# Kernel tuning notes

Hardware: AMD Instinct MI355X
Metric: run time of the kernel (lower is better)

## Reference

```python
import jax, jax.numpy as jnp
import numpy as np

LEAK = 0.9
BASE_THRESH = 1.0
BN_EPS = 1e-5

@jax.custom_vjp
def spike_fn(x):
    return (x >= 0).astype(x.dtype)

def _spike_fwd(x):
    return (x >= 0).astype(x.dtype), x

def _spike_bwd(x, g):
    return (g / (1.0 + 5.0 * jnp.abs(x)) ** 2,)

spike_fn.defvjp(_spike_fwd, _spike_bwd)


def setup_inputs() -> dict:
    key = jax.random.key(0)
    ks = jax.random.split(key, 8)
    B, T, C, H, NC, DT = 256, 2048, 64, 64, 4, 50
    kin_spikes_seq = jax.random.normal(ks[0], (B, T, C), dtype=jnp.float32)
    tda_features = jax.random.normal(ks[1], (B, DT), dtype=jnp.float32)
    # spatial_conv1x1: Linear(64 -> 64, bias=False); weight [out, in]
    W_spatial = jax.random.normal(ks[2], (H, C), dtype=jnp.float32) / np.sqrt(C)
    bn_gamma = jnp.ones((H,), dtype=jnp.float32)
    bn_beta = jnp.zeros((H,), dtype=jnp.float32)
    # class_conv1x1: Linear(64 -> 4, bias=False)
    W_class = jax.random.normal(ks[3], (NC, H), dtype=jnp.float32) / np.sqrt(H)
    lateral = jnp.eye(NC, dtype=jnp.float32) * 0.8 - 0.1
    # tda_to_thresh: Linear(50 -> 4)
    W_tda = jax.random.normal(ks[4], (NC, DT), dtype=jnp.float32) / np.sqrt(DT)
    b_tda = jnp.zeros((NC,), dtype=jnp.float32)
    return {
        "kin_spikes_seq": kin_spikes_seq,
        "tda_features": tda_features,
        "W_spatial": W_spatial,
        "bn_gamma": bn_gamma,
        "bn_beta": bn_beta,
        "W_class": W_class,
        "lateral": lateral,
        "W_tda": W_tda,
        "b_tda": b_tda,
    }


def reference(kin_spikes_seq, tda_features, W_spatial, bn_gamma, bn_beta,
              W_class, lateral, W_tda, b_tda):
    # [B, T, C] @ [C, H] -> [B, T, H]
    x_proj = jnp.einsum("btc,hc->bth", kin_spikes_seq, W_spatial)
    # BatchNorm1d in training mode: per-channel stats over (B, T)
    mean = jnp.mean(x_proj, axis=(0, 1))
    var = jnp.var(x_proj, axis=(0, 1))
    x_proj = (x_proj - mean) * jax.lax.rsqrt(var + BN_EPS) * bn_gamma + bn_beta

    tda_mod = jax.nn.sigmoid(tda_features @ W_tda.T + b_tda) * 0.5  # [B, 4]
    dynamic_thresh = BASE_THRESH + tda_mod

    B = kin_spikes_seq.shape[0]
    H, NC = W_class.shape[1], W_class.shape[0]
    mem1 = jnp.zeros((B, H), dtype=x_proj.dtype)
    mem2 = jnp.zeros((B, NC), dtype=x_proj.dtype)
    spike_sum = jnp.zeros((B, NC), dtype=x_proj.dtype)

    def step(carry, xt):
        mem1, mem2, ssum = carry
        mem1 = LEAK * mem1 + xt
        spk1 = spike_fn(mem1 - BASE_THRESH)
        mem1 = mem1 * (1.0 - spk1)
        cur2 = (spk1 @ W_class.T) @ lateral  # [B, 4]
        mem2 = LEAK * mem2 + cur2
        spk2 = spike_fn(mem2 - dynamic_thresh)
        mem2 = mem2 * (1.0 - spk2)
        return (mem1, mem2, ssum + spk2), None

    xs = jnp.swapaxes(x_proj, 0, 1)  # [T, B, H]
    (mem1, mem2, spike_sum), _ = jax.lax.scan(step, (mem1, mem2, spike_sum), xs)
    return spike_sum
```

## Files before the change

### kernel.cpp

```cpp
#include <hip/hip_runtime.h>
#include <cstdint>
#include <cstddef>
#include <cmath>

#define BB 256
#define TB 2048
#define NROWS (BB*TB)
#define R1 256
#define NBLK_K1 (NROWS/R1)
#define NBLK1 4096

typedef float f32x4 __attribute__((ext_vector_type(4)));
typedef float f32x2 __attribute__((ext_vector_type(2)));

#define OFF_X      0ull
#define SZ_X       ((size_t)NROWS*64*4)
#define OFF_PART   (OFF_X + SZ_X)
#define SZ_PART    ((size_t)128*NBLK1*4)
#define OFF_STAT   (OFF_PART + SZ_PART)
#define SZ_STAT    (128*8)

__global__ __launch_bounds__(256, 2) void k1_gemm(const float* __restrict__ kin,
                                                  const float* __restrict__ Wsp,
                                                  float* __restrict__ xproj,
                                                  float* __restrict__ partials) {
  __shared__ float4 As[R1 * 16];
  __shared__ f32x4 Wp[32 * 32];
  const int tid = threadIdx.x;
  const int ty = tid >> 3;
  const int tx = tid & 7;
  const size_t r0 = (size_t)blockIdx.x * R1;

  const f32x4* kin4 = (const f32x4*)(kin + r0 * 64);
  #pragma unroll
  for (int k = 0; k < 16; ++k) {
    int idx = k * 256 + tid;
    int r = idx >> 4, cc = idx & 15;
    f32x4 v = __builtin_nontemporal_load(&kin4[idx]);
    As[r * 16 + (cc ^ ((r >> 3) & 7))] = make_float4(v.x, v.y, v.z, v.w);
  }
  #pragma unroll
  for (int k = 0; k < 4; ++k) {
    int idx = k * 256 + tid;
    int p = idx >> 5, q = idx & 31;
    float2 w0 = *(const float2*)(Wsp + (2 * p) * 64 + 2 * q);
    float2 w1 = *(const float2*)(Wsp + (2 * p + 1) * 64 + 2 * q);
    Wp[p * 32 + (q ^ ((p >> 2) & 7))] = (f32x4){w0.x, w1.x, w0.y, w1.y};
  }
  __syncthreads();

  f32x2 acc2[8][4];
  #pragma unroll
  for (int i = 0; i < 8; ++i)
    #pragma unroll
    for (int jp = 0; jp < 4; ++jp) acc2[i][jp] = (f32x2){0.f, 0.f};

  #pragma unroll 1
  for (int cc = 0; cc < 16; ++cc) {
    float4 av[8];
    f32x4 q0[4], q1[4];
    #pragma unroll
    for (int i = 0; i < 8; ++i)
      av[i] = As[(8 * ty + i) * 16 + (cc ^ (ty & 7))];
    #pragma unroll
    for (int jp = 0; jp < 4; ++jp) {
      const int p = 4 * tx + jp;
      q0[jp] = Wp[p * 32 + ((2 * cc)     ^ tx)];
      q1[jp] = Wp[p * 32 + ((2 * cc + 1) ^ tx)];
    }
    #pragma unroll
    for (int i = 0; i < 8; ++i) {
      #pragma unroll
      for (int jp = 0; jp < 4; ++jp) {
        acc2[i][jp] = __builtin_elementwise_fma((f32x2){av[i].x, av[i].x}, q0[jp].xy, acc2[i][jp]);
        acc2[i][jp] = __builtin_elementwise_fma((f32x2){av[i].y, av[i].y}, q0[jp].zw, acc2[i][jp]);
        acc2[i][jp] = __builtin_elementwise_fma((f32x2){av[i].z, av[i].z}, q1[jp].xy, acc2[i][jp]);
        acc2[i][jp] = __builtin_elementwise_fma((f32x2){av[i].w, av[i].w}, q1[jp].zw, acc2[i][jp]);
      }
    }
  }

  #pragma unroll
  for (int i = 0; i < 8; ++i) {
    const size_t row = r0 + 8 * ty + i;
    f32x4 lo = {acc2[i][0].x, acc2[i][0].y, acc2[i][1].x, acc2[i][1].y};
    f32x4 hi = {acc2[i][2].x, acc2[i][2].y, acc2[i][3].x, acc2[i][3].y};
    *(f32x4*)(xproj + row * 64 + 8 * tx)     = lo;
    *(f32x4*)(xproj + row * 64 + 8 * tx + 4) = hi;
  }

  __syncthreads();
  float* Sm = (float*)As;
  float* Sq = Sm + 64 * 33;
  #pragma unroll
  for (int j = 0; j < 8; ++j) {
    const int col = 8 * tx + j;
    float s = 0.f, q = 0.f;
    #pragma unroll
    for (int i = 0; i < 8; ++i) {
      float v = (j & 1) ? acc2[i][j >> 1].y : acc2[i][j >> 1].x;
      s += v;
      q += v * v;
    }
    Sm[col * 33 + ty] = s;
    Sq[col * 33 + ty] = q;
  }
  __syncthreads();
  if (tid < 64) {
    float s0 = 0.f, q0 = 0.f, s1 = 0.f, q1 = 0.f;
    #pragma unroll
    for (int g = 0; g < 16; ++g)  { s0 += Sm[tid * 33 + g]; q0 += Sq[tid * 33 + g]; }
    #pragma unroll
    for (int g = 16; g < 32; ++g) { s1 += Sm[tid * 33 + g]; q1 += Sq[tid * 33 + g]; }
    const size_t p0 = 2 * (size_t)blockIdx.x;
    partials[(size_t)tid * NBLK1 + p0]            = s0;
    partials[(size_t)tid * NBLK1 + p0 + 1]        = s1;
    partials[(size_t)(64 + tid) * NBLK1 + p0]     = q0;
    partials[(size_t)(64 + tid) * NBLK1 + p0 + 1] = q1;
  }
}

__global__ __launch_bounds__(256) void k2a_reduce(const float* __restrict__ partials,
                                                  double* __restrict__ statd) {
  __shared__ double sd[256];
  const int idx = blockIdx.x;
  double acc = 0.0;
  for (int k = threadIdx.x; k < NBLK1; k += 256)
    acc += (double)partials[(size_t)idx * NBLK1 + k];
  sd[threadIdx.x] = acc;
  __syncthreads();
  for (int s = 128; s > 0; s >>= 1) {
    if (threadIdx.x < s) sd[threadIdx.x] += sd[threadIdx.x + s];
    __syncthreads();
  }
  if (threadIdx.x == 0) statd[idx] = sd[0];
}

#define K3_LOAD(BUF, TBASE)                         \
  { _Pragma("unroll") for (int i_ = 0; i_ < 64; ++i_) \
      BUF[i_] = xr[(size_t)((TBASE) + i_) * 64]; }

#define K3_CHUNK(CUR, NXT0, TBASE)                                   \
  { unsigned long long keep = 0;                                     \
    _Pragma("unroll") for (int i_ = 0; i_ < 64; ++i_) {              \
      bool sp = (mem >= 1.0f);                                       \
      unsigned long long mb = __ballot(sp);                          \
      if (h == i_) keep = mb;                                        \
      float xrn = (i_ < 63) ? CUR[(i_ + 1) & 63] : (NXT0);           \
      float xn = fmaf(xrn, sc, sh);                                  \
      mem = sp ? xn : fmaf(mem, 0.9f, xn);                           \
    }                                                                \
    masksL[(TBASE) + h] = keep; }

#define K45_LOAD(BUF, TBASE)                                             \
  { _Pragma("unroll") for (int k_ = 0; k_ < 16; ++k_) {                  \
      f32x4 v = *(const f32x4*)(cr + (TBASE) + 4 * k_);                  \
      BUF[4 * k_] = v.x; BUF[4 * k_ + 1] = v.y;                          \
      BUF[4 * k_ + 2] = v.z; BUF[4 * k_ + 3] = v.w; } }

#define K45_CHUNK(CUR, NXT0)                                  \
  { _Pragma("unroll") for (int i_ = 0; i_ < 64; ++i_) {       \
      bool sp = (mem2 >= th);                                 \
      cnt += sp ? 1u : 0u;                                    \
      float xn = (i_ < 63) ? CUR[(i_ + 1) & 63] : (NXT0);     \
      mem2 = sp ? xn : fmaf(mem2, 0.9f, xn);                  \
    } }

__global__ __launch_bounds__(256) void k345_scan(const float* __restrict__ xproj,
                                                 const double* __restrict__ statd,
                                                 const float* __restrict__ gamma,
                                                 const float* __restrict__ beta,
                                                 const float* __restrict__ Wc,
                                                 const float* __restrict__ lat,
                                                 const float* __restrict__ tda,
                                                 const float* __restrict__ Wtda,
                                                 const float* __restrict__ btda,
                                                 float* __restrict__ out) {
  __shared__ unsigned long long masksL[TB];
  __shared__ float WcL[256];
  __shared__ float latL[16];
  __shared__ float thL[4];
  __shared__ float lbuf[4][TB + 4];
  const int tid = threadIdx.x, b = blockIdx.x;

  WcL[tid] = Wc[tid];
  if (tid < 16) latL[tid] = lat[tid];

  if (tid < 64) {
    const int h = tid;
    const double mean = statd[h] / (double)NROWS;
    const double ex2  = statd[64 + h] / (double)NROWS;
    const double var  = ex2 - mean * mean;
    const double scd  = (double)gamma[h] / sqrt(var + 1e-5);
    const float sc = (float)scd;
    const float sh = (float)((double)beta[h] - mean * scd);

    const float* xr = xproj + (size_t)b * TB * 64 + h;
    float xa[64], xb[64];

    K3_LOAD(xa, 0)
    float mem = fmaf(xa[0], sc, sh);

    #pragma unroll 1
    for (int t0 = 0; t0 < TB; t0 += 128) {
      K3_LOAD(xb, t0 + 64)
      K3_CHUNK(xa, xb[0], t0)
      if (t0 + 128 < TB) { K3_LOAD(xa, t0 + 128) }
      K3_CHUNK(xb, xa[0], t0 + 64)
    }
  } else if (tid < 68) {
    const int j = tid - 64;
    double acc = (double)btda[j];
    for (int k = 0; k < 50; ++k)
      acc += (double)tda[b * 50 + k] * (double)Wtda[j * 50 + k];
    double sig = 1.0 / (1.0 + exp(-acc));
    thL[j] = (float)(1.0 + 0.5 * sig);
  }
  __syncthreads();

  #pragma unroll 1
  for (int c = 0; c < 8; ++c) {
    const int t = c * 256 + tid;
    const unsigned long long m = masksL[t];
    const unsigned lo = (unsigned)m, hi = (unsigned)(m >> 32);
    float v0 = 0.f, v1 = 0.f, v2 = 0.f, v3 = 0.f;
    #pragma unroll
    for (int hh = 0; hh < 32; ++hh) {
      const float bit = (float)((lo >> hh) & 1u);
      v0 = fmaf(bit, WcL[hh],       v0);
      v1 = fmaf(bit, WcL[64 + hh],  v1);
      v2 = fmaf(bit, WcL[128 + hh], v2);
      v3 = fmaf(bit, WcL[192 + hh], v3);
    }
    #pragma unroll
    for (int hh = 32; hh < 64; ++hh) {
      const float bit = (float)((hi >> (hh - 32)) & 1u);
      v0 = fmaf(bit, WcL[hh],       v0);
      v1 = fmaf(bit, WcL[64 + hh],  v1);
      v2 = fmaf(bit, WcL[128 + hh], v2);
      v3 = fmaf(bit, WcL[192 + hh], v3);
    }
    { float cx = v0 * latL[0];  cx = fmaf(v1, latL[4],  cx); cx = fmaf(v2, latL[8],  cx); cx = fmaf(v3, latL[12], cx); lbuf[0][t] = cx; }
    { float cx = v0 * latL[1];  cx = fmaf(v1, latL[5],  cx); cx = fmaf(v2, latL[9],  cx); cx = fmaf(v3, latL[13], cx); lbuf[1][t] = cx; }
    { float cx = v0 * latL[2];  cx = fmaf(v1, latL[6],  cx); cx = fmaf(v2, latL[10], cx); cx = fmaf(v3, latL[14], cx); lbuf[2][t] = cx; }
    { float cx = v0 * latL[3];  cx = fmaf(v1, latL[7],  cx); cx = fmaf(v2, latL[11], cx); cx = fmaf(v3, latL[15], cx); lbuf[3][t] = cx; }
  }
  __syncthreads();
  if (tid >= 64) return;

  const int j4 = tid & 3;
  const float th = thL[j4];
  const float* cr = lbuf[j4];
  float ca[64], cb[64];

  K45_LOAD(ca, 0)
  float mem2 = ca[0];
  unsigned cnt = 0;

  #pragma unroll 1
  for (int t0 = 0; t0 < TB; t0 += 128) {
    K45_LOAD(cb, t0 + 64)
    K45_CHUNK(ca, cb[0])
    if (t0 + 128 < TB) { K45_LOAD(ca, t0 + 128) }
    K45_CHUNK(cb, ca[0])
  }
  if (tid < 4) out[b * 4 + j4] = (float)cnt;
}

extern "C" void kernel_launch(void* const* d_in, const int* in_sizes, int n_in,
                              void* d_out, int out_size, void* d_ws, size_t ws_size,
                              hipStream_t stream) {
  const float* kin   = (const float*)d_in[0];
  const float* tda   = (const float*)d_in[1];
  const float* Wsp   = (const float*)d_in[2];
  const float* gamma = (const float*)d_in[3];
  const float* beta  = (const float*)d_in[4];
  const float* Wc    = (const float*)d_in[5];
  const float* lat   = (const float*)d_in[6];
  const float* Wtda  = (const float*)d_in[7];
  const float* btda  = (const float*)d_in[8];

  char* ws = (char*)d_ws;
  float*  xproj    = (float*)(ws + OFF_X);
  float*  partials = (float*)(ws + OFF_PART);
  double* statd    = (double*)(ws + OFF_STAT);
  float*  out      = (float*)d_out;

  k1_gemm  <<<dim3(NBLK_K1), dim3(256), 0, stream>>>(kin, Wsp, xproj, partials);
  k2a_reduce<<<dim3(128),  dim3(256), 0, stream>>>(partials, statd);
  k345_scan<<<dim3(BB),    dim3(256), 0, stream>>>(xproj, statd, gamma, beta,
                                                   Wc, lat, tda, Wtda, btda, out);
}
```

Measured before the change: 157.0 us.

## Stage xproj chunks through swizzled LDS with producer waves feeding the scan wave

The layer-1 membrane scan is split into a producer/consumer pipeline. Waves 1-3 issue coalesced vector loads of 64-timestep chunks of xproj and write them transposed into a 4-deep, XOR-swizzled LDS ring. Wave 0 reads rows from LDS and runs the serial spike recurrence, with a block barrier after every chunk. This replaces the old strided per-lane global loads with latency hidden by coalesced prefetch, at the cost of 64 KB extra LDS (lower occupancy) and 32 block barriers.

```diff
diff --git a/kernel.cpp b/kernel.cpp
--- a/kernel.cpp
+++ b/kernel.cpp
@@ -136,22 +136,6 @@
   if (threadIdx.x == 0) statd[idx] = sd[0];
 }
 
-#define K3_LOAD(BUF, TBASE)                         \
-  { _Pragma("unroll") for (int i_ = 0; i_ < 64; ++i_) \
-      BUF[i_] = xr[(size_t)((TBASE) + i_) * 64]; }
-
-#define K3_CHUNK(CUR, NXT0, TBASE)                                   \
-  { unsigned long long keep = 0;                                     \
-    _Pragma("unroll") for (int i_ = 0; i_ < 64; ++i_) {              \
-      bool sp = (mem >= 1.0f);                                       \
-      unsigned long long mb = __ballot(sp);                          \
-      if (h == i_) keep = mb;                                        \
-      float xrn = (i_ < 63) ? CUR[(i_ + 1) & 63] : (NXT0);           \
-      float xn = fmaf(xrn, sc, sh);                                  \
-      mem = sp ? xn : fmaf(mem, 0.9f, xn);                           \
-    }                                                                \
-    masksL[(TBASE) + h] = keep; }
-
 #define K45_LOAD(BUF, TBASE)                                             \
   { _Pragma("unroll") for (int k_ = 0; k_ < 16; ++k_) {                  \
       f32x4 v = *(const f32x4*)(cr + (TBASE) + 4 * k_);                  \
@@ -165,6 +149,23 @@
       float xn = (i_ < 63) ? CUR[(i_ + 1) & 63] : (NXT0);     \
       mem2 = sp ? xn : fmaf(mem2, 0.9f, xn);                  \
     } }
+
+#define PROD_WRITE(BF)                                                        \
+  { _Pragma("unroll") for (int h2 = 0; h2 < 64; ++h2) {                       \
+      float pv;                                                               \
+      switch (h2 & 3) {                                                       \
+        case 0: pv = pregs[h2 >> 2].x; break;                                 \
+        case 1: pv = pregs[h2 >> 2].y; break;                                 \
+        case 2: pv = pregs[h2 >> 2].z; break;                                 \
+        default: pv = pregs[h2 >> 2].w; break;                                \
+      }                                                                       \
+      xs[BF][h2][4 * ((lane >> 2) ^ (h2 & 7)) + (lane & 3)] = pv;             \
+    } }
+
+#define PROD_ISSUE(C)                                                         \
+  { const f32x4* xr_ = (const f32x4*)(xproj + ((size_t)b * TB +               \
+                                      (size_t)(C) * 64 + lane) * 64);         \
+    _Pragma("unroll") for (int k_ = 0; k_ < 16; ++k_) pregs[k_] = xr_[k_]; }
 
 __global__ __launch_bounds__(256) void k345_scan(const float* __restrict__ xproj,
                                                  const double* __restrict__ statd,
@@ -176,45 +177,88 @@
                                                  const float* __restrict__ Wtda,
                                                  const float* __restrict__ btda,
                                                  float* __restrict__ out) {
+  __shared__ float xs[4][64][64];
   __shared__ unsigned long long masksL[TB];
   __shared__ float WcL[256];
   __shared__ float latL[16];
   __shared__ float thL[4];
   __shared__ float lbuf[4][TB + 4];
   const int tid = threadIdx.x, b = blockIdx.x;
+  const int lane = tid & 63;
+  const int wv = tid >> 6;
 
   WcL[tid] = Wc[tid];
   if (tid < 16) latL[tid] = lat[tid];
 
-  if (tid < 64) {
-    const int h = tid;
+  float sc = 0.f, sh = 0.f, mem = 0.f;
+  f32x4 pregs[16];
+
+  if (wv == 1 || wv == 2) {
+    const int c = wv - 1;
+    PROD_ISSUE(c)
+    PROD_WRITE(c)
+  } else if (wv == 3) {
+    if (lane < 4) {
+      const int j = lane;
+      double acc = (double)btda[j];
+      for (int k = 0; k < 50; ++k)
+        acc += (double)tda[b * 50 + k] * (double)Wtda[j * 50 + k];
+      double sig = 1.0 / (1.0 + exp(-acc));
+      thL[j] = (float)(1.0 + 0.5 * sig);
+    }
+  } else {
+    const int h = lane;
     const double mean = statd[h] / (double)NROWS;
     const double ex2  = statd[64 + h] / (double)NROWS;
     const double var  = ex2 - mean * mean;
     const double scd  = (double)gamma[h] / sqrt(var + 1e-5);
-    const float sc = (float)scd;
-    const float sh = (float)((double)beta[h] - mean * scd);
-
-    const float* xr = xproj + (size_t)b * TB * 64 + h;
-    float xa[64], xb[64];
-
-    K3_LOAD(xa, 0)
-    float mem = fmaf(xa[0], sc, sh);
-
-    #pragma unroll 1
-    for (int t0 = 0; t0 < TB; t0 += 128) {
-      K3_LOAD(xb, t0 + 64)
-      K3_CHUNK(xa, xb[0], t0)
-      if (t0 + 128 < TB) { K3_LOAD(xa, t0 + 128) }
-      K3_CHUNK(xb, xa[0], t0 + 64)
-    }
-  } else if (tid < 68) {
-    const int j = tid - 64;
-    double acc = (double)btda[j];
-    for (int k = 0; k < 50; ++k)
-      acc += (double)tda[b * 50 + k] * (double)Wtda[j * 50 + k];
-    double sig = 1.0 / (1.0 + exp(-acc));
-    thL[j] = (float)(1.0 + 0.5 * sig);
+    sc = (float)scd;
+    sh = (float)((double)beta[h] - mean * scd);
+  }
+  __syncthreads();
+
+  if (wv == 3) { PROD_ISSUE(2) }
+  else if (wv == 1) { PROD_ISSUE(3) }
+  else if (wv == 0) {
+    mem = fmaf(xs[0][lane][4 * (lane & 7)], sc, sh);
+  }
+
+  #pragma unroll 1
+  for (int n = 0; n < 32; ++n) {
+    if (n + 2 < 32 && wv == 1 + ((n + 2) % 3)) {
+      const int bf = (n + 2) & 3;
+      PROD_WRITE(bf)
+    }
+    if (n + 4 < 32 && wv == 1 + ((n + 1) % 3)) {
+      PROD_ISSUE(n + 4)
+    }
+    if (wv == 0) {
+      const int bf = n & 3, swz = lane & 7;
+      const float4* xrow = (const float4*)&xs[bf][lane][0];
+      float4 v4[16];
+      #pragma unroll
+      for (int i = 0; i < 16; ++i) v4[i] = xrow[i ^ swz];
+      float vv[64];
+      #pragma unroll
+      for (int i = 0; i < 16; ++i) {
+        vv[4*i] = v4[i].x; vv[4*i+1] = v4[i].y; vv[4*i+2] = v4[i].z; vv[4*i+3] = v4[i].w;
+      }
+      const float nxt0 = (n < 31) ? xs[(n + 1) & 3][lane][4 * swz] : 0.f;
+      unsigned long long keep = 0ull;
+      #pragma unroll
+      for (int i_ = 0; i_ < 64; ++i_) {
+        bool sp = (mem >= 1.0f);
+        unsigned long long mb = __ballot(sp);
+        if (lane == i_) keep = mb;
+        float xrn = (i_ < 63) ? vv[(i_ + 1) & 63] : nxt0;
+        float xn = fmaf(xrn, sc, sh);
+        mem = sp ? xn : fmaf(mem, 0.9f, xn);
+      }
+      masksL[n * 64 + lane] = keep;
+    }
+    asm volatile("s_waitcnt lgkmcnt(0)" ::: "memory");
+    __builtin_amdgcn_sched_barrier(0);
+    __builtin_amdgcn_s_barrier();
   }
   __syncthreads();
 
```

Result: faster. 150.7 us (-4.0%).
